# Performance work log

Measured on AMD Instinct MI355X. Metric: run time of the kernel, lower is better.

The kernel has to match this reference:

```python
import jax, jax.numpy as jnp
import numpy as np

DIM = 1024
HID = 4096
E = 8
K = 3


def setup_inputs() -> dict:
    key = jax.random.key(0)
    ks = jax.random.split(key, 5)
    x = jax.random.normal(ks[0], (2, 2048, DIM), dtype=jnp.float32)
    # router: nn.Linear(dim, E) -- initialized to zero in source, but we use small
    # random weights so routing is non-degenerate for the correctness baseline.
    router_w = jax.random.normal(ks[1], (E, DIM), dtype=jnp.float32) * 0.02
    router_b = jax.random.normal(ks[2], (E,), dtype=jnp.float32) * 0.02
    # per-expert SwiGLU params: w12: [E, dim, 2*hid], w3: [E, hid, dim]
    w12 = jax.random.normal(ks[3], (E, DIM, 2 * HID), dtype=jnp.float32) * 0.02
    w3 = jax.random.normal(ks[4], (E, HID, DIM), dtype=jnp.float32) * 0.02
    return {"x": x, "router_w": router_w, "router_b": router_b, "w12": w12, "w3": w3}


def _moe(x, router_w, router_b, w12, w3):
    # router logits [B, S, E]
    logits = jnp.einsum("bsd,ed->bse", x, router_w) + router_b
    scores = jax.nn.sigmoid(logits)
    topk_scores, topk_idx = jax.lax.top_k(scores, K)  # [B,S,K]
    weights = topk_scores / (topk_scores.sum(axis=-1, keepdims=True) + 1e-6)
    # dense per-expert combine weight [B, S, E] (zero if expert not selected)
    onehot = jax.nn.one_hot(topk_idx, E, dtype=x.dtype)  # [B,S,K,E]
    dense_w = jnp.einsum("bske,bsk->bse", onehot, weights)
    out = jnp.zeros_like(x)
    for e in range(E):  # small fixed structural loop over experts
        x12 = x @ w12[e]  # [B,S,2H]
        x1, x2 = jnp.split(x12, 2, axis=-1)
        hidden = jax.nn.silu(x1) * x2
        out = out + (hidden @ w3[e]) * dense_w[..., e:e + 1]
    aux_loss = 0.01 * jnp.mean(logits ** 2)
    return out, aux_loss


def reference(x, router_w, router_b, w12, w3):
    return _moe(x, router_w, router_b, w12, w3)
```

## Files before the change

kernel.cpp:

```cpp
#include <hip/hip_runtime.h>
#include <math.h>

typedef unsigned short u16;
typedef __bf16 bf16x8 __attribute__((ext_vector_type(8)));
typedef float f32x4 __attribute__((ext_vector_type(4)));

#define T_TOK 4096
#define DIM   1024
#define HID   4096
#define NE    8
#define TOPK  3
#define NPAIR 12288

constexpr size_t OFF_CTRL = 0;
constexpr size_t OFF_XB   = 256;
constexpr size_t OFF_W12T = OFF_XB   + (size_t)T_TOK * DIM * 2;
constexpr size_t OFF_W3T  = OFF_W12T + (size_t)NE * 2 * HID * DIM * 2;
constexpr size_t OFF_HID  = OFF_W3T  + (size_t)NE * DIM * HID * 2;
constexpr size_t OFF_Y    = OFF_HID  + (size_t)NPAIR * HID * 2;
constexpr size_t OFF_PTOK = OFF_Y    + (size_t)NPAIR * DIM * 4;
constexpr size_t OFF_TE   = OFF_PTOK + (size_t)NPAIR * 4;
constexpr size_t OFF_TW   = OFF_TE   + (size_t)T_TOK * TOPK * 4;
constexpr size_t OFF_TS   = OFF_TW   + (size_t)T_TOK * TOPK * 4;

__device__ __forceinline__ u16 f2bf(float f) {
    unsigned u = __builtin_bit_cast(unsigned, f);
    u += 0x7fffu + ((u >> 16) & 1u);
    return (u16)(u >> 16);
}

__device__ __forceinline__ void ld_g2l(const u16* g, u16* l) {
    __builtin_amdgcn_global_load_lds((__attribute__((address_space(1))) unsigned*)(g),
                                     (__attribute__((address_space(3))) unsigned*)(l),
                                     16, 0, 0);
}

__global__ __launch_bounds__(256) void transpose_cast_kernel(const float* __restrict__ in,
                                                             u16* __restrict__ out, int K, int N) {
    __shared__ float tile[64][33];
    const float* inp = in + (size_t)blockIdx.z * K * N;
    u16* outp = out + (size_t)blockIdx.z * K * N;
    const int n0 = blockIdx.x * 32, k0 = blockIdx.y * 64;
    const int tid = threadIdx.x;
#pragma unroll
    for (int i = 0; i < 2; ++i) {
        int k = i * 32 + (tid >> 3);
        int c4 = (tid & 7) * 4;
        float4 f = *(const float4*)(inp + (size_t)(k0 + k) * N + n0 + c4);
        tile[k][c4 + 0] = f.x; tile[k][c4 + 1] = f.y;
        tile[k][c4 + 2] = f.z; tile[k][c4 + 3] = f.w;
    }
    __syncthreads();
    const int n = tid >> 3, c = (tid & 7) * 8;
    u16 buf[8];
#pragma unroll
    for (int j = 0; j < 8; ++j) buf[j] = f2bf(tile[c + j][n]);
    *(uint4*)(outp + (size_t)(n0 + n) * K + k0 + c) = *(uint4*)buf;
}

__global__ __launch_bounds__(256) void router_kernel(const float* __restrict__ x,
                                                     const float* __restrict__ rw,
                                                     const float* __restrict__ rb,
                                                     u16* __restrict__ xb,
                                                     int* __restrict__ tok_expert,
                                                     float* __restrict__ tok_w,
                                                     int* __restrict__ ctrl,
                                                     float* __restrict__ aux) {
    __shared__ int hist[NE];
    __shared__ float auxsh;
    const int tid = threadIdx.x;
    if (tid < NE) hist[tid] = 0;
    if (tid == NE) auxsh = 0.f;
    __syncthreads();

    const int wave = tid >> 6, lane = tid & 63;
    const int t = blockIdx.x * 4 + wave;
    const float* xr = x + (size_t)t * DIM;
    u16* xbr = xb + (size_t)t * DIM;

    float p[NE];
#pragma unroll
    for (int e = 0; e < NE; e++) p[e] = 0.f;
#pragma unroll
    for (int q = 0; q < 4; ++q) {
        const int d = q * 256 + lane * 4;
        float4 f = *(const float4*)(xr + d);
        uint2 v;
        v.x = (unsigned)f2bf(f.x) | ((unsigned)f2bf(f.y) << 16);
        v.y = (unsigned)f2bf(f.z) | ((unsigned)f2bf(f.w) << 16);
        *(uint2*)(xbr + d) = v;
#pragma unroll
        for (int e = 0; e < NE; e++) {
            float4 w = *(const float4*)(rw + e * DIM + d);
            p[e] += f.x * w.x + f.y * w.y + f.z * w.z + f.w * w.w;
        }
    }
#pragma unroll
    for (int e = 0; e < NE; e++) {
#pragma unroll
        for (int off = 32; off; off >>= 1) p[e] += __shfl_down(p[e], off, 64);
    }
    if (lane == 0) {
        float s[NE]; float auxs = 0.f;
#pragma unroll
        for (int e = 0; e < NE; e++) {
            float lg = p[e] + rb[e];
            auxs += lg * lg;
            s[e] = 1.f / (1.f + __expf(-lg));
        }
        atomicAdd(&auxsh, auxs);
        unsigned mask = 0; float wsum = 0.f;
        int idxs[TOPK]; float vals[TOPK];
        for (int k = 0; k < TOPK; k++) {
            float best = -1.f; int bi = 0;
            for (int e = 0; e < NE; e++)
                if (!((mask >> e) & 1u) && s[e] > best) { best = s[e]; bi = e; }
            mask |= 1u << bi; idxs[k] = bi; vals[k] = best; wsum += best;
        }
        wsum += 1e-6f;
        for (int k = 0; k < TOPK; k++) {
            tok_expert[t * TOPK + k] = idxs[k];
            tok_w[t * TOPK + k] = vals[k] / wsum;
            atomicAdd(&hist[idxs[k]], 1);
        }
    }
    __syncthreads();
    if (tid < NE) { int h = hist[tid]; if (h) atomicAdd(&ctrl[tid], h); }
    if (tid == NE) atomicAdd(aux, auxsh * (0.01f / 32768.0f));
}

__global__ void scan_kernel(int* __restrict__ ctrl) {
    if (threadIdx.x == 0) {
        int acc = 0;
        for (int e = 0; e < NE; e++) { ctrl[8 + e] = acc; acc += ctrl[e]; }
    }
}

__global__ __launch_bounds__(256) void assign_kernel(const int* __restrict__ tok_expert,
                                                     const float* __restrict__ tok_w,
                                                     int* __restrict__ ctrl,
                                                     int* __restrict__ pair_token,
                                                     int* __restrict__ tok_slot) {
    int t = blockIdx.x * blockDim.x + threadIdx.x;
    if (t >= T_TOK) return;
    for (int k = 0; k < TOPK; k++) {
        int e = tok_expert[t * TOPK + k];
        int pos = atomicAdd(&ctrl[16 + e], 1);
        int slot = ctrl[8 + e] + pos;
        pair_token[slot] = t;
        tok_slot[t * TOPK + k] = slot;
    }
}

__global__ __launch_bounds__(256, 3) void gemm1_kernel(const u16* __restrict__ xb,
                                                       const u16* __restrict__ w12t,
                                                       const int* __restrict__ pair_token,
                                                       const int* __restrict__ ctrl,
                                                       u16* __restrict__ hidden) {
    const int e = blockIdx.z;
    const int cnt = ctrl[e];
    if ((int)blockIdx.y * 128 >= cnt) return;
    const int off = ctrl[8 + e];
    const int rowbase = off + blockIdx.y * 128;
    const int rowend = off + cnt;
    const int n0 = blockIdx.x * 64;

    __shared__ __align__(16) u16 Alds[128 * 64];
    __shared__ __align__(16) u16 B0lds[64 * 64];
    __shared__ __align__(16) u16 B1lds[64 * 64];

    const int tid = threadIdx.x;
    const int wave = tid >> 6, lane = tid & 63;
    const int lr8 = lane >> 3;
    const int lc  = (lane & 7) ^ lr8;

    const u16* srcA[4];
    const u16* srcB0[2];
    const u16* srcB1[2];
#pragma unroll
    for (int g = 0; g < 4; ++g) {
        int sr = rowbase + wave * 32 + g * 8 + lr8;
        int tok = (sr < rowend) ? pair_token[sr] : 0;
        srcA[g] = xb + (size_t)tok * DIM + lc * 8;
    }
#pragma unroll
    for (int g = 0; g < 2; ++g) {
        int br = n0 + wave * 16 + g * 8 + lr8;
        srcB0[g] = w12t + ((size_t)e * 2 * HID + br) * DIM + lc * 8;
        srcB1[g] = srcB0[g] + (size_t)HID * DIM;
    }

    const int wm = wave >> 1, wn = wave & 1;
    const int lrow = lane & 15, lq = lane >> 4;
    const int xm = lrow & 7;

    f32x4 acc0[4][2], acc1[4][2];
#pragma unroll
    for (int mf = 0; mf < 4; mf++)
#pragma unroll
        for (int nf = 0; nf < 2; nf++) { acc0[mf][nf] = (f32x4)0.f; acc1[mf][nf] = (f32x4)0.f; }

    for (int kt = 0; kt < DIM / 64; ++kt) {
#pragma unroll
        for (int g = 0; g < 4; ++g)
            ld_g2l(srcA[g], Alds + (wave * 32 + g * 8) * 64);
#pragma unroll
        for (int g = 0; g < 2; ++g) {
            ld_g2l(srcB0[g], B0lds + (wave * 16 + g * 8) * 64);
            ld_g2l(srcB1[g], B1lds + (wave * 16 + g * 8) * 64);
        }
#pragma unroll
        for (int g = 0; g < 4; ++g) srcA[g] += 64;
#pragma unroll
        for (int g = 0; g < 2; ++g) { srcB0[g] += 64; srcB1[g] += 64; }
        __syncthreads();
#pragma unroll
        for (int kk = 0; kk < 2; ++kk) {
            const int so = (((kk << 2) | lq) ^ xm) * 8;
            bf16x8 a[4], b0[2], b1[2];
#pragma unroll
            for (int mf = 0; mf < 4; mf++)
                a[mf] = *(const bf16x8*)(Alds + (wm * 64 + mf * 16 + lrow) * 64 + so);
#pragma unroll
            for (int nf = 0; nf < 2; nf++) {
                b0[nf] = *(const bf16x8*)(B0lds + (wn * 32 + nf * 16 + lrow) * 64 + so);
                b1[nf] = *(const bf16x8*)(B1lds + (wn * 32 + nf * 16 + lrow) * 64 + so);
            }
#pragma unroll
            for (int mf = 0; mf < 4; mf++)
#pragma unroll
                for (int nf = 0; nf < 2; nf++) {
                    acc0[mf][nf] = __builtin_amdgcn_mfma_f32_16x16x32_bf16(a[mf], b0[nf], acc0[mf][nf], 0, 0, 0);
                    acc1[mf][nf] = __builtin_amdgcn_mfma_f32_16x16x32_bf16(a[mf], b1[nf], acc1[mf][nf], 0, 0, 0);
                }
        }
        __syncthreads();
    }
#pragma unroll
    for (int mf = 0; mf < 4; mf++)
#pragma unroll
        for (int nf = 0; nf < 2; nf++) {
            const int gc = n0 + wn * 32 + nf * 16 + lrow;
#pragma unroll
            for (int r = 0; r < 4; r++) {
                const int gr = rowbase + wm * 64 + mf * 16 + lq * 4 + r;
                if (gr < rowend) {
                    float x1 = acc0[mf][nf][r], x2 = acc1[mf][nf][r];
                    float h = x1 / (1.f + __expf(-x1)) * x2;
                    hidden[(size_t)gr * HID + gc] = f2bf(h);
                }
            }
        }
}

__global__ __launch_bounds__(256, 3) void gemm2_kernel(const u16* __restrict__ hidden,
                                                       const u16* __restrict__ w3t,
                                                       const int* __restrict__ ctrl,
                                                       float* __restrict__ ybuf) {
    const int e = blockIdx.z;
    const int cnt = ctrl[e];
    if ((int)blockIdx.y * 128 >= cnt) return;
    const int off = ctrl[8 + e];
    const int rowbase = off + blockIdx.y * 128;
    const int rowend = off + cnt;
    const int n0 = blockIdx.x * 128;

    __shared__ __align__(16) u16 Alds[128 * 64];
    __shared__ __align__(16) u16 Blds[128 * 64];

    const int tid = threadIdx.x;
    const int wave = tid >> 6, lane = tid & 63;
    const int lr8 = lane >> 3;
    const int lc  = (lane & 7) ^ lr8;

    const u16* srcA[4];
    const u16* srcB[4];
#pragma unroll
    for (int g = 0; g < 4; ++g) {
        int sr = rowbase + wave * 32 + g * 8 + lr8;
        if (sr > NPAIR - 1) sr = NPAIR - 1;
        srcA[g] = hidden + (size_t)sr * HID + lc * 8;
        int br = n0 + wave * 32 + g * 8 + lr8;
        srcB[g] = w3t + ((size_t)e * DIM + br) * HID + lc * 8;
    }

    const int wm = wave >> 1, wn = wave & 1;
    const int lrow = lane & 15, lq = lane >> 4;
    const int xm = lrow & 7;

    f32x4 acc[4][4];
#pragma unroll
    for (int mf = 0; mf < 4; mf++)
#pragma unroll
        for (int nf = 0; nf < 4; nf++) acc[mf][nf] = (f32x4)0.f;

    for (int kt = 0; kt < HID / 64; ++kt) {
#pragma unroll
        for (int g = 0; g < 4; ++g) {
            ld_g2l(srcA[g], Alds + (wave * 32 + g * 8) * 64);
            ld_g2l(srcB[g], Blds + (wave * 32 + g * 8) * 64);
        }
#pragma unroll
        for (int g = 0; g < 4; ++g) { srcA[g] += 64; srcB[g] += 64; }
        __syncthreads();
#pragma unroll
        for (int kk = 0; kk < 2; ++kk) {
            const int so = (((kk << 2) | lq) ^ xm) * 8;
            bf16x8 a[4], b[4];
#pragma unroll
            for (int mf = 0; mf < 4; mf++)
                a[mf] = *(const bf16x8*)(Alds + (wm * 64 + mf * 16 + lrow) * 64 + so);
#pragma unroll
            for (int nf = 0; nf < 4; nf++)
                b[nf] = *(const bf16x8*)(Blds + (wn * 64 + nf * 16 + lrow) * 64 + so);
#pragma unroll
            for (int mf = 0; mf < 4; mf++)
#pragma unroll
                for (int nf = 0; nf < 4; nf++)
                    acc[mf][nf] = __builtin_amdgcn_mfma_f32_16x16x32_bf16(a[mf], b[nf], acc[mf][nf], 0, 0, 0);
        }
        __syncthreads();
    }
#pragma unroll
    for (int mf = 0; mf < 4; mf++)
#pragma unroll
        for (int nf = 0; nf < 4; nf++) {
            const int gc = n0 + wn * 64 + nf * 16 + lrow;
#pragma unroll
            for (int r = 0; r < 4; r++) {
                const int gr = rowbase + wm * 64 + mf * 16 + lq * 4 + r;
                if (gr < rowend) ybuf[(size_t)gr * DIM + gc] = acc[mf][nf][r];
            }
        }
}

__global__ __launch_bounds__(256) void combine_kernel(const float* __restrict__ ybuf,
                                                      const int* __restrict__ tok_slot,
                                                      const float* __restrict__ tok_w,
                                                      float* __restrict__ out) {
    const int t = blockIdx.x;
    const int d = threadIdx.x * 4;
    const int s0 = tok_slot[t * 3 + 0], s1 = tok_slot[t * 3 + 1], s2 = tok_slot[t * 3 + 2];
    const float w0 = tok_w[t * 3 + 0], w1 = tok_w[t * 3 + 1], w2 = tok_w[t * 3 + 2];
    const float4 a0 = *(const float4*)(ybuf + (size_t)s0 * DIM + d);
    const float4 a1 = *(const float4*)(ybuf + (size_t)s1 * DIM + d);
    const float4 a2 = *(const float4*)(ybuf + (size_t)s2 * DIM + d);
    float4 o;
    o.x = w0 * a0.x + w1 * a1.x + w2 * a2.x;
    o.y = w0 * a0.y + w1 * a1.y + w2 * a2.y;
    o.z = w0 * a0.z + w1 * a1.z + w2 * a2.z;
    o.w = w0 * a0.w + w1 * a1.w + w2 * a2.w;
    *(float4*)(out + (size_t)t * DIM + d) = o;
}

extern "C" void kernel_launch(void* const* d_in, const int* in_sizes, int n_in,
                              void* d_out, int out_size, void* d_ws, size_t ws_size,
                              hipStream_t stream) {
    const float* x   = (const float*)d_in[0];
    const float* rw  = (const float*)d_in[1];
    const float* rb  = (const float*)d_in[2];
    const float* w12 = (const float*)d_in[3];
    const float* w3  = (const float*)d_in[4];
    float* out = (float*)d_out;
    char* ws = (char*)d_ws;

    int*   ctrl       = (int*)(ws + OFF_CTRL);
    u16*   xb         = (u16*)(ws + OFF_XB);
    u16*   w12t       = (u16*)(ws + OFF_W12T);
    u16*   w3t        = (u16*)(ws + OFF_W3T);
    u16*   hidden     = (u16*)(ws + OFF_HID);
    float* ybuf       = (float*)(ws + OFF_Y);
    int*   pair_token = (int*)(ws + OFF_PTOK);
    int*   tok_expert = (int*)(ws + OFF_TE);
    float* tok_w      = (float*)(ws + OFF_TW);
    int*   tok_slot   = (int*)(ws + OFF_TS);

    hipMemsetAsync(ctrl, 0, 256, stream);
    hipMemsetAsync(out + (size_t)T_TOK * DIM, 0, sizeof(float), stream);

    router_kernel<<<T_TOK / 4, 256, 0, stream>>>(x, rw, rb, xb, tok_expert, tok_w, ctrl,
                                                 out + (size_t)T_TOK * DIM);
    transpose_cast_kernel<<<dim3(2 * HID / 32, DIM / 64, NE), 256, 0, stream>>>(w12, w12t, DIM, 2 * HID);
    transpose_cast_kernel<<<dim3(DIM / 32, HID / 64, NE), 256, 0, stream>>>(w3, w3t, HID, DIM);
    scan_kernel<<<1, 64, 0, stream>>>(ctrl);
    assign_kernel<<<16, 256, 0, stream>>>(tok_expert, tok_w, ctrl, pair_token, tok_slot);

    gemm1_kernel<<<dim3(HID / 64, 32, NE), 256, 0, stream>>>(xb, w12t, pair_token, ctrl, hidden);
    gemm2_kernel<<<dim3(DIM / 128, 32, NE), 256, 0, stream>>>(hidden, w3t, ctrl, ybuf);
    combine_kernel<<<T_TOK, 256, 0, stream>>>(ybuf, tok_slot, tok_w, out);
    (void)in_sizes; (void)n_in; (void)out_size; (void)ws_size;
}
```

Baseline: 989.6 us.

## Rewrite expert GEMMs with 256-row tiles, double-buffered LDS and ping-pong scheduling

Both grouped GEMMs move to 512-thread blocks with 256x128 and 256x256 output tiles. They stage operands into double-buffered dynamic LDS, so global-to-LDS loads for the next K tile overlap the MFMA work on the current one. The inner loop is split into quadrants with explicit barriers, waitcnts, sched_barriers and s_setprio to interleave LDS reads and MFMA issue across waves. Larger tiles raise data reuse, but they waste more rows at uneven expert boundaries, use 128KB of LDS per block and give fewer blocks per expert.

```diff
diff --git a/kernel.cpp b/kernel.cpp
--- a/kernel.cpp
+++ b/kernel.cpp
@@ -34,6 +34,23 @@
                                      (__attribute__((address_space(3))) unsigned*)(l),
                                      16, 0, 0);
 }
+
+#define VMCNT0 asm volatile("s_waitcnt vmcnt(0)" ::: "memory")
+#define LGKM0  asm volatile("s_waitcnt lgkmcnt(0)" ::: "memory")
+#define SBAR   __builtin_amdgcn_s_barrier()
+#define SCHED0 __builtin_amdgcn_sched_barrier(0)
+
+#define STAGE8(dst)                                                    \
+  {                                                                    \
+    _Pragma("unroll")                                                  \
+    for (int r_ = 0; r_ < 4; ++r_)                                     \
+      ld_g2l(srcA[r_], (dst) + (r_ * 64 + wave * 8) * 64);             \
+    _Pragma("unroll")                                                  \
+    for (int r_ = 0; r_ < 4; ++r_)                                     \
+      ld_g2l(srcB[r_], (dst) + 16384 + (r_ * 64 + wave * 8) * 64);     \
+    _Pragma("unroll")                                                  \
+    for (int r_ = 0; r_ < 4; ++r_) { srcA[r_] += 64; srcB[r_] += 64; } \
+  }
 
 __global__ __launch_bounds__(256) void transpose_cast_kernel(const float* __restrict__ in,
                                                              u16* __restrict__ out, int K, int N) {
@@ -152,98 +169,140 @@
     }
 }
 
-__global__ __launch_bounds__(256, 3) void gemm1_kernel(const u16* __restrict__ xb,
+__global__ __launch_bounds__(512, 2) void gemm1_kernel(const u16* __restrict__ xb,
                                                        const u16* __restrict__ w12t,
                                                        const int* __restrict__ pair_token,
                                                        const int* __restrict__ ctrl,
                                                        u16* __restrict__ hidden) {
     const int e = blockIdx.z;
     const int cnt = ctrl[e];
-    if ((int)blockIdx.y * 128 >= cnt) return;
+    if ((int)blockIdx.y * 256 >= cnt) return;
     const int off = ctrl[8 + e];
-    const int rowbase = off + blockIdx.y * 128;
+    const int rowbase = off + blockIdx.y * 256;
     const int rowend = off + cnt;
-    const int n0 = blockIdx.x * 64;
-
-    __shared__ __align__(16) u16 Alds[128 * 64];
-    __shared__ __align__(16) u16 B0lds[64 * 64];
-    __shared__ __align__(16) u16 B1lds[64 * 64];
+    const int n0 = blockIdx.x * 128;
+
+    extern __shared__ __align__(16) u16 lds[];
 
     const int tid = threadIdx.x;
     const int wave = tid >> 6, lane = tid & 63;
-    const int lr8 = lane >> 3;
-    const int lc  = (lane & 7) ^ lr8;
+    const int srow = tid >> 3;
+    const int scol = ((tid & 7) ^ (srow & 7)) * 8;
 
     const u16* srcA[4];
-    const u16* srcB0[2];
-    const u16* srcB1[2];
-#pragma unroll
-    for (int g = 0; g < 4; ++g) {
-        int sr = rowbase + wave * 32 + g * 8 + lr8;
+    const u16* srcB[4];
+#pragma unroll
+    for (int r = 0; r < 4; ++r) {
+        int sr = rowbase + r * 64 + srow;
         int tok = (sr < rowend) ? pair_token[sr] : 0;
-        srcA[g] = xb + (size_t)tok * DIM + lc * 8;
-    }
-#pragma unroll
-    for (int g = 0; g < 2; ++g) {
-        int br = n0 + wave * 16 + g * 8 + lr8;
-        srcB0[g] = w12t + ((size_t)e * 2 * HID + br) * DIM + lc * 8;
-        srcB1[g] = srcB0[g] + (size_t)HID * DIM;
-    }
-
-    const int wm = wave >> 1, wn = wave & 1;
-    const int lrow = lane & 15, lq = lane >> 4;
-    const int xm = lrow & 7;
-
-    f32x4 acc0[4][2], acc1[4][2];
-#pragma unroll
-    for (int mf = 0; mf < 4; mf++)
-#pragma unroll
-        for (int nf = 0; nf < 2; nf++) { acc0[mf][nf] = (f32x4)0.f; acc1[mf][nf] = (f32x4)0.f; }
-
-    for (int kt = 0; kt < DIM / 64; ++kt) {
-#pragma unroll
-        for (int g = 0; g < 4; ++g)
-            ld_g2l(srcA[g], Alds + (wave * 32 + g * 8) * 64);
-#pragma unroll
-        for (int g = 0; g < 2; ++g) {
-            ld_g2l(srcB0[g], B0lds + (wave * 16 + g * 8) * 64);
-            ld_g2l(srcB1[g], B1lds + (wave * 16 + g * 8) * 64);
-        }
-#pragma unroll
-        for (int g = 0; g < 4; ++g) srcA[g] += 64;
-#pragma unroll
-        for (int g = 0; g < 2; ++g) { srcB0[g] += 64; srcB1[g] += 64; }
-        __syncthreads();
-#pragma unroll
-        for (int kk = 0; kk < 2; ++kk) {
-            const int so = (((kk << 2) | lq) ^ xm) * 8;
-            bf16x8 a[4], b0[2], b1[2];
-#pragma unroll
-            for (int mf = 0; mf < 4; mf++)
-                a[mf] = *(const bf16x8*)(Alds + (wm * 64 + mf * 16 + lrow) * 64 + so);
-#pragma unroll
-            for (int nf = 0; nf < 2; nf++) {
-                b0[nf] = *(const bf16x8*)(B0lds + (wn * 32 + nf * 16 + lrow) * 64 + so);
-                b1[nf] = *(const bf16x8*)(B1lds + (wn * 32 + nf * 16 + lrow) * 64 + so);
-            }
-#pragma unroll
-            for (int mf = 0; mf < 4; mf++)
-#pragma unroll
-                for (int nf = 0; nf < 2; nf++) {
-                    acc0[mf][nf] = __builtin_amdgcn_mfma_f32_16x16x32_bf16(a[mf], b0[nf], acc0[mf][nf], 0, 0, 0);
-                    acc1[mf][nf] = __builtin_amdgcn_mfma_f32_16x16x32_bf16(a[mf], b1[nf], acc1[mf][nf], 0, 0, 0);
-                }
-        }
-        __syncthreads();
-    }
-#pragma unroll
-    for (int mf = 0; mf < 4; mf++)
-#pragma unroll
-        for (int nf = 0; nf < 2; nf++) {
+        srcA[r] = xb + (size_t)tok * DIM + scol;
+    }
+#pragma unroll
+    for (int r = 0; r < 2; ++r) {
+        srcB[r]     = w12t + ((size_t)e * 2 * HID + n0 + r * 64 + srow) * DIM + scol;
+        srcB[r + 2] = srcB[r] + (size_t)HID * DIM;
+    }
+
+    const int wm = wave >> 2, wn = wave & 3;
+    const int lrow = lane & 15, lq = lane >> 4, xm = lrow & 7;
+    const int so0 = ((lq ^ xm) << 3);
+    const int so1 = (((4 | lq) ^ xm) << 3);
+
+    f32x4 acc0[8][2], acc1[8][2];
+#pragma unroll
+    for (int mf = 0; mf < 8; ++mf)
+#pragma unroll
+        for (int nf = 0; nf < 2; ++nf) { acc0[mf][nf] = (f32x4)0.f; acc1[mf][nf] = (f32x4)0.f; }
+
+    STAGE8(lds);
+    VMCNT0; SBAR;
+
+    for (int kt = 0; kt < 16; ++kt) {
+        u16* sl = lds + (kt & 1) * 32768;
+        u16* sn = lds + ((kt & 1) ^ 1) * 32768;
+        const u16* sA = sl;
+        const u16* sB = sl + 16384;
+        if (kt < 15) STAGE8(sn);
+
+        bf16x8 a[4][2], b0[2][2], b1[2][2];
+#pragma unroll
+        for (int mf = 0; mf < 4; ++mf) {
+            const u16* base = sA + (wm * 128 + mf * 16 + lrow) * 64;
+            a[mf][0] = *(const bf16x8*)(base + so0);
+            a[mf][1] = *(const bf16x8*)(base + so1);
+        }
+#pragma unroll
+        for (int nf = 0; nf < 2; ++nf) {
+            const u16* base = sB + (wn * 32 + nf * 16 + lrow) * 64;
+            b0[nf][0] = *(const bf16x8*)(base + so0);
+            b0[nf][1] = *(const bf16x8*)(base + so1);
+        }
+        SBAR; LGKM0; SCHED0;
+        __builtin_amdgcn_s_setprio(1);
+#pragma unroll
+        for (int mf = 0; mf < 4; ++mf)
+#pragma unroll
+            for (int nf = 0; nf < 2; ++nf) {
+                acc0[mf][nf] = __builtin_amdgcn_mfma_f32_16x16x32_bf16(a[mf][0], b0[nf][0], acc0[mf][nf], 0, 0, 0);
+                acc0[mf][nf] = __builtin_amdgcn_mfma_f32_16x16x32_bf16(a[mf][1], b0[nf][1], acc0[mf][nf], 0, 0, 0);
+            }
+        __builtin_amdgcn_s_setprio(0);
+        SBAR;
+#pragma unroll
+        for (int nf = 0; nf < 2; ++nf) {
+            const u16* base = sB + 128 * 64 + (wn * 32 + nf * 16 + lrow) * 64;
+            b1[nf][0] = *(const bf16x8*)(base + so0);
+            b1[nf][1] = *(const bf16x8*)(base + so1);
+        }
+        SBAR; LGKM0; SCHED0;
+        __builtin_amdgcn_s_setprio(1);
+#pragma unroll
+        for (int mf = 0; mf < 4; ++mf)
+#pragma unroll
+            for (int nf = 0; nf < 2; ++nf) {
+                acc1[mf][nf] = __builtin_amdgcn_mfma_f32_16x16x32_bf16(a[mf][0], b1[nf][0], acc1[mf][nf], 0, 0, 0);
+                acc1[mf][nf] = __builtin_amdgcn_mfma_f32_16x16x32_bf16(a[mf][1], b1[nf][1], acc1[mf][nf], 0, 0, 0);
+            }
+        __builtin_amdgcn_s_setprio(0);
+        SBAR;
+#pragma unroll
+        for (int mf = 0; mf < 4; ++mf) {
+            const u16* base = sA + (wm * 128 + (mf + 4) * 16 + lrow) * 64;
+            a[mf][0] = *(const bf16x8*)(base + so0);
+            a[mf][1] = *(const bf16x8*)(base + so1);
+        }
+        SBAR; LGKM0; SCHED0;
+        __builtin_amdgcn_s_setprio(1);
+#pragma unroll
+        for (int mf = 0; mf < 4; ++mf)
+#pragma unroll
+            for (int nf = 0; nf < 2; ++nf) {
+                acc1[mf + 4][nf] = __builtin_amdgcn_mfma_f32_16x16x32_bf16(a[mf][0], b1[nf][0], acc1[mf + 4][nf], 0, 0, 0);
+                acc1[mf + 4][nf] = __builtin_amdgcn_mfma_f32_16x16x32_bf16(a[mf][1], b1[nf][1], acc1[mf + 4][nf], 0, 0, 0);
+            }
+        __builtin_amdgcn_s_setprio(0);
+        SBAR;
+        __builtin_amdgcn_s_setprio(1);
+#pragma unroll
+        for (int mf = 0; mf < 4; ++mf)
+#pragma unroll
+            for (int nf = 0; nf < 2; ++nf) {
+                acc0[mf + 4][nf] = __builtin_amdgcn_mfma_f32_16x16x32_bf16(a[mf][0], b0[nf][0], acc0[mf + 4][nf], 0, 0, 0);
+                acc0[mf + 4][nf] = __builtin_amdgcn_mfma_f32_16x16x32_bf16(a[mf][1], b0[nf][1], acc0[mf + 4][nf], 0, 0, 0);
+            }
+        __builtin_amdgcn_s_setprio(0);
+        VMCNT0; SBAR;
+    }
+
+#pragma unroll
+    for (int mf = 0; mf < 8; ++mf) {
+        const int gr0 = rowbase + wm * 128 + mf * 16 + lq * 4;
+#pragma unroll
+        for (int nf = 0; nf < 2; ++nf) {
             const int gc = n0 + wn * 32 + nf * 16 + lrow;
 #pragma unroll
-            for (int r = 0; r < 4; r++) {
-                const int gr = rowbase + wm * 64 + mf * 16 + lq * 4 + r;
+            for (int r = 0; r < 4; ++r) {
+                const int gr = gr0 + r;
                 if (gr < rowend) {
                     float x1 = acc0[mf][nf][r], x2 = acc1[mf][nf][r];
                     float h = x1 / (1.f + __expf(-x1)) * x2;
@@ -251,87 +310,142 @@
                 }
             }
         }
-}
-
-__global__ __launch_bounds__(256, 3) void gemm2_kernel(const u16* __restrict__ hidden,
+    }
+}
+
+__global__ __launch_bounds__(512, 2) void gemm2_kernel(const u16* __restrict__ hidden,
                                                        const u16* __restrict__ w3t,
                                                        const int* __restrict__ ctrl,
                                                        float* __restrict__ ybuf) {
     const int e = blockIdx.z;
     const int cnt = ctrl[e];
-    if ((int)blockIdx.y * 128 >= cnt) return;
+    if ((int)blockIdx.y * 256 >= cnt) return;
     const int off = ctrl[8 + e];
-    const int rowbase = off + blockIdx.y * 128;
+    const int rowbase = off + blockIdx.y * 256;
     const int rowend = off + cnt;
-    const int n0 = blockIdx.x * 128;
-
-    __shared__ __align__(16) u16 Alds[128 * 64];
-    __shared__ __align__(16) u16 Blds[128 * 64];
+    const int n0 = blockIdx.x * 256;
+
+    extern __shared__ __align__(16) u16 lds[];
 
     const int tid = threadIdx.x;
     const int wave = tid >> 6, lane = tid & 63;
-    const int lr8 = lane >> 3;
-    const int lc  = (lane & 7) ^ lr8;
+    const int srow = tid >> 3;
+    const int scol = ((tid & 7) ^ (srow & 7)) * 8;
 
     const u16* srcA[4];
     const u16* srcB[4];
 #pragma unroll
-    for (int g = 0; g < 4; ++g) {
-        int sr = rowbase + wave * 32 + g * 8 + lr8;
+    for (int r = 0; r < 4; ++r) {
+        int sr = rowbase + r * 64 + srow;
         if (sr > NPAIR - 1) sr = NPAIR - 1;
-        srcA[g] = hidden + (size_t)sr * HID + lc * 8;
-        int br = n0 + wave * 32 + g * 8 + lr8;
-        srcB[g] = w3t + ((size_t)e * DIM + br) * HID + lc * 8;
-    }
-
-    const int wm = wave >> 1, wn = wave & 1;
-    const int lrow = lane & 15, lq = lane >> 4;
-    const int xm = lrow & 7;
-
-    f32x4 acc[4][4];
-#pragma unroll
-    for (int mf = 0; mf < 4; mf++)
-#pragma unroll
-        for (int nf = 0; nf < 4; nf++) acc[mf][nf] = (f32x4)0.f;
-
-    for (int kt = 0; kt < HID / 64; ++kt) {
-#pragma unroll
-        for (int g = 0; g < 4; ++g) {
-            ld_g2l(srcA[g], Alds + (wave * 32 + g * 8) * 64);
-            ld_g2l(srcB[g], Blds + (wave * 32 + g * 8) * 64);
-        }
-#pragma unroll
-        for (int g = 0; g < 4; ++g) { srcA[g] += 64; srcB[g] += 64; }
-        __syncthreads();
-#pragma unroll
-        for (int kk = 0; kk < 2; ++kk) {
-            const int so = (((kk << 2) | lq) ^ xm) * 8;
-            bf16x8 a[4], b[4];
-#pragma unroll
-            for (int mf = 0; mf < 4; mf++)
-                a[mf] = *(const bf16x8*)(Alds + (wm * 64 + mf * 16 + lrow) * 64 + so);
-#pragma unroll
-            for (int nf = 0; nf < 4; nf++)
-                b[nf] = *(const bf16x8*)(Blds + (wn * 64 + nf * 16 + lrow) * 64 + so);
-#pragma unroll
-            for (int mf = 0; mf < 4; mf++)
-#pragma unroll
-                for (int nf = 0; nf < 4; nf++)
-                    acc[mf][nf] = __builtin_amdgcn_mfma_f32_16x16x32_bf16(a[mf], b[nf], acc[mf][nf], 0, 0, 0);
-        }
-        __syncthreads();
-    }
-#pragma unroll
-    for (int mf = 0; mf < 4; mf++)
-#pragma unroll
-        for (int nf = 0; nf < 4; nf++) {
+        srcA[r] = hidden + (size_t)sr * HID + scol;
+        srcB[r] = w3t + ((size_t)e * DIM + n0 + r * 64 + srow) * HID + scol;
+    }
+
+    const int wm = wave >> 2, wn = wave & 3;
+    const int lrow = lane & 15, lq = lane >> 4, xm = lrow & 7;
+    const int so0 = ((lq ^ xm) << 3);
+    const int so1 = (((4 | lq) ^ xm) << 3);
+
+    f32x4 acc[8][4];
+#pragma unroll
+    for (int mf = 0; mf < 8; ++mf)
+#pragma unroll
+        for (int nf = 0; nf < 4; ++nf) acc[mf][nf] = (f32x4)0.f;
+
+    STAGE8(lds);
+    VMCNT0; SBAR;
+
+    for (int kt = 0; kt < 64; ++kt) {
+        u16* sl = lds + (kt & 1) * 32768;
+        u16* sn = lds + ((kt & 1) ^ 1) * 32768;
+        const u16* sA = sl;
+        const u16* sB = sl + 16384;
+        if (kt < 63) STAGE8(sn);
+
+        bf16x8 a[4][2], b[4][2];
+#pragma unroll
+        for (int mf = 0; mf < 4; ++mf) {
+            const u16* base = sA + (wm * 128 + mf * 16 + lrow) * 64;
+            a[mf][0] = *(const bf16x8*)(base + so0);
+            a[mf][1] = *(const bf16x8*)(base + so1);
+        }
+#pragma unroll
+        for (int nf = 0; nf < 2; ++nf) {
+            const u16* base = sB + (wn * 64 + nf * 16 + lrow) * 64;
+            b[nf][0] = *(const bf16x8*)(base + so0);
+            b[nf][1] = *(const bf16x8*)(base + so1);
+        }
+        SBAR; LGKM0; SCHED0;
+        __builtin_amdgcn_s_setprio(1);
+#pragma unroll
+        for (int mf = 0; mf < 4; ++mf)
+#pragma unroll
+            for (int nf = 0; nf < 2; ++nf) {
+                acc[mf][nf] = __builtin_amdgcn_mfma_f32_16x16x32_bf16(a[mf][0], b[nf][0], acc[mf][nf], 0, 0, 0);
+                acc[mf][nf] = __builtin_amdgcn_mfma_f32_16x16x32_bf16(a[mf][1], b[nf][1], acc[mf][nf], 0, 0, 0);
+            }
+        __builtin_amdgcn_s_setprio(0);
+        SBAR;
+#pragma unroll
+        for (int nf = 2; nf < 4; ++nf) {
+            const u16* base = sB + (wn * 64 + nf * 16 + lrow) * 64;
+            b[nf][0] = *(const bf16x8*)(base + so0);
+            b[nf][1] = *(const bf16x8*)(base + so1);
+        }
+        SBAR; LGKM0; SCHED0;
+        __builtin_amdgcn_s_setprio(1);
+#pragma unroll
+        for (int mf = 0; mf < 4; ++mf)
+#pragma unroll
+            for (int nf = 2; nf < 4; ++nf) {
+                acc[mf][nf] = __builtin_amdgcn_mfma_f32_16x16x32_bf16(a[mf][0], b[nf][0], acc[mf][nf], 0, 0, 0);
+                acc[mf][nf] = __builtin_amdgcn_mfma_f32_16x16x32_bf16(a[mf][1], b[nf][1], acc[mf][nf], 0, 0, 0);
+            }
+        __builtin_amdgcn_s_setprio(0);
+        SBAR;
+#pragma unroll
+        for (int mf = 0; mf < 4; ++mf) {
+            const u16* base = sA + (wm * 128 + (mf + 4) * 16 + lrow) * 64;
+            a[mf][0] = *(const bf16x8*)(base + so0);
+            a[mf][1] = *(const bf16x8*)(base + so1);
+        }
+        SBAR; LGKM0; SCHED0;
+        __builtin_amdgcn_s_setprio(1);
+#pragma unroll
+        for (int mf = 0; mf < 4; ++mf)
+#pragma unroll
+            for (int nf = 2; nf < 4; ++nf) {
+                acc[mf + 4][nf] = __builtin_amdgcn_mfma_f32_16x16x32_bf16(a[mf][0], b[nf][0], acc[mf + 4][nf], 0, 0, 0);
+                acc[mf + 4][nf] = __builtin_amdgcn_mfma_f32_16x16x32_bf16(a[mf][1], b[nf][1], acc[mf + 4][nf], 0, 0, 0);
+            }
+        __builtin_amdgcn_s_setprio(0);
+        SBAR;
+        __builtin_amdgcn_s_setprio(1);
+#pragma unroll
+        for (int mf = 0; mf < 4; ++mf)
+#pragma unroll
+            for (int nf = 0; nf < 2; ++nf) {
+                acc[mf + 4][nf] = __builtin_amdgcn_mfma_f32_16x16x32_bf16(a[mf][0], b[nf][0], acc[mf + 4][nf], 0, 0, 0);
+                acc[mf + 4][nf] = __builtin_amdgcn_mfma_f32_16x16x32_bf16(a[mf][1], b[nf][1], acc[mf + 4][nf], 0, 0, 0);
+            }
+        __builtin_amdgcn_s_setprio(0);
+        VMCNT0; SBAR;
+    }
+
+#pragma unroll
+    for (int mf = 0; mf < 8; ++mf) {
+        const int gr0 = rowbase + wm * 128 + mf * 16 + lq * 4;
+#pragma unroll
+        for (int nf = 0; nf < 4; ++nf) {
             const int gc = n0 + wn * 64 + nf * 16 + lrow;
 #pragma unroll
-            for (int r = 0; r < 4; r++) {
-                const int gr = rowbase + wm * 64 + mf * 16 + lq * 4 + r;
+            for (int r = 0; r < 4; ++r) {
+                const int gr = gr0 + r;
                 if (gr < rowend) ybuf[(size_t)gr * DIM + gc] = acc[mf][nf][r];
             }
         }
+    }
 }
 
 __global__ __launch_bounds__(256) void combine_kernel(const float* __restrict__ ybuf,
@@ -375,6 +489,13 @@
     float* tok_w      = (float*)(ws + OFF_TW);
     int*   tok_slot   = (int*)(ws + OFF_TS);
 
+    static bool attr_set = false;
+    if (!attr_set) {
+        hipFuncSetAttribute((const void*)gemm1_kernel, hipFuncAttributeMaxDynamicSharedMemorySize, 131072);
+        hipFuncSetAttribute((const void*)gemm2_kernel, hipFuncAttributeMaxDynamicSharedMemorySize, 131072);
+        attr_set = true;
+    }
+
     hipMemsetAsync(ctrl, 0, 256, stream);
     hipMemsetAsync(out + (size_t)T_TOK * DIM, 0, sizeof(float), stream);
 
@@ -385,8 +506,8 @@
     scan_kernel<<<1, 64, 0, stream>>>(ctrl);
     assign_kernel<<<16, 256, 0, stream>>>(tok_expert, tok_w, ctrl, pair_token, tok_slot);
 
-    gemm1_kernel<<<dim3(HID / 64, 32, NE), 256, 0, stream>>>(xb, w12t, pair_token, ctrl, hidden);
-    gemm2_kernel<<<dim3(DIM / 128, 32, NE), 256, 0, stream>>>(hidden, w3t, ctrl, ybuf);
+    gemm1_kernel<<<dim3(HID / 128, 16, NE), 512, 131072, stream>>>(xb, w12t, pair_token, ctrl, hidden);
+    gemm2_kernel<<<dim3(DIM / 256, 16, NE), 512, 131072, stream>>>(hidden, w3t, ctrl, ybuf);
     combine_kernel<<<T_TOK, 256, 0, stream>>>(ybuf, tok_slot, tok_w, out);
     (void)in_sizes; (void)n_in; (void)out_size; (void)ws_size;
 }
```

Result: faster. 964.8 us (-2.5%).
